# Performance work log

Hardware: AMD Instinct MI355X
Metric: run time of the kernel (lower is better)

## Reference

```python
import jax, jax.numpy as jnp
import numpy as np

B, S, T, DIN, DM, H = 4, 2048, 2048, 256, 512, 8
DH = DM // H
NEG = float(-2**32 + 1)
EPS = 1e-6


def layer_norm(x, g, b):
    mu = jnp.mean(x, axis=-1, keepdims=True)
    var = jnp.mean(jnp.square(x - mu), axis=-1, keepdims=True)
    return (x - mu) * jax.lax.rsqrt(var + EPS) * g + b


def mha(q_in, k_in, v_in, key_mask, wq, bq, wk, bk, wv, bv, w2, b2, g, beta, masked):
    b_, sq, _ = q_in.shape
    sk = k_in.shape[1]
    Q = (q_in @ wq + bq).reshape(b_, sq, H, DH)
    K = (k_in @ wk + bk).reshape(b_, sk, H, DH)
    V = (v_in @ wv + bv).reshape(b_, sk, H, DH)
    scores = jnp.einsum('bqhd,bkhd->bhqk', Q, K) / jnp.sqrt(jnp.float32(DH))
    if masked:
        m = key_mask.astype(jnp.float32).reshape(b_, 1, 1, sk)  # [B,1,1,Tk]
        scores = jnp.where(m == 0, jnp.float32(NEG), scores)
    attn = jax.nn.softmax(scores, axis=-1)  # dropout = identity at inference
    out = jnp.einsum('bhqk,bkhd->bqhd', attn, V).reshape(b_, sq, DM)
    out = out @ w2 + b2 + q_in
    return layer_norm(out, g, beta)


def setup_inputs() -> dict:
    key = jax.random.key(0)
    ks = jax.random.split(key, 16)
    w = lambda k, shp: (jax.random.normal(k, shp, jnp.float32) * 0.02)
    d = {
        'x': jax.random.normal(ks[0], (B, S, DIN), jnp.float32),
        'encoder_output': jax.random.normal(ks[1], (B, T, DIN), jnp.float32),
        'tgt_mask': jax.random.randint(ks[2], (B, S, 1), 0, 2, jnp.int32),
        'src_mask': jax.random.randint(ks[3], (B, T, 1), 0, 2, jnp.int32),
        'm1_wq': w(ks[4], (DIN, DM)), 'm1_bq': jnp.zeros((DM,), jnp.float32),
        'm1_wk': w(ks[5], (DIN, DM)), 'm1_bk': jnp.zeros((DM,), jnp.float32),
        'm1_wv': w(ks[6], (DIN, DM)), 'm1_bv': jnp.zeros((DM,), jnp.float32),
        'm1_w2': w(ks[7], (DM, DIN)), 'm1_b2': jnp.zeros((DIN,), jnp.float32),
        'm1_g': jnp.ones((DIN,), jnp.float32), 'm1_b': jnp.zeros((DIN,), jnp.float32),
        'm2_wq': w(ks[8], (DIN, DM)), 'm2_bq': jnp.zeros((DM,), jnp.float32),
        'm2_wk': w(ks[9], (DIN, DM)), 'm2_bk': jnp.zeros((DM,), jnp.float32),
        'm2_wv': w(ks[10], (DIN, DM)), 'm2_bv': jnp.zeros((DM,), jnp.float32),
        'm2_w2': w(ks[11], (DM, DIN)), 'm2_b2': jnp.zeros((DIN,), jnp.float32),
        'm2_g': jnp.ones((DIN,), jnp.float32), 'm2_b': jnp.zeros((DIN,), jnp.float32),
        'ln1_g': jnp.ones((DIN,), jnp.float32), 'ln1_b': jnp.zeros((DIN,), jnp.float32),
        'ln2_g': jnp.ones((DIN,), jnp.float32), 'ln2_b': jnp.zeros((DIN,), jnp.float32),
        'ln3_g': jnp.ones((DIN,), jnp.float32), 'ln3_b': jnp.zeros((DIN,), jnp.float32),
        'ffn_w1': w(ks[12], (DIN, DM)), 'ffn_b1': jnp.zeros((DM,), jnp.float32),
        'ffn_w2': w(ks[13], (DM, DIN)), 'ffn_b2': jnp.zeros((DIN,), jnp.float32),
    }
    return d


def reference(x, encoder_output, tgt_mask, src_mask,
              m1_wq, m1_bq, m1_wk, m1_bk, m1_wv, m1_bv, m1_w2, m1_b2, m1_g, m1_b,
              m2_wq, m2_bq, m2_wk, m2_bk, m2_wv, m2_bv, m2_w2, m2_b2, m2_g, m2_b,
              ln1_g, ln1_b, ln2_g, ln2_b, ln3_g, ln3_b,
              ffn_w1, ffn_b1, ffn_w2, ffn_b2):
    attn1 = mha(x, x, x, tgt_mask, m1_wq, m1_bq, m1_wk, m1_bk, m1_wv, m1_bv,
                m1_w2, m1_b2, m1_g, m1_b, masked=True)
    x = layer_norm(x + attn1, ln1_g, ln1_b)
    attn2 = mha(x, encoder_output, encoder_output, src_mask,
                m2_wq, m2_bq, m2_wk, m2_bk, m2_wv, m2_bv,
                m2_w2, m2_b2, m2_g, m2_b, masked=False)
    x = layer_norm(x + attn2, ln2_g, ln2_b)
    ffn_out = jax.nn.relu(x @ ffn_w1 + ffn_b1) @ ffn_w2 + ffn_b2
    return layer_norm(x + ffn_out, ln3_g, ln3_b)
```

## Files before the change

### kernel.cpp

```cpp
#include <hip/hip_runtime.h>
#include <hip/hip_bf16.h>

#define B_ 4
#define S_ 2048
#define DIN_ 256
#define DM_ 512
#define H_ 8
#define DH_ 64
#define M_ (B_*S_)

typedef short bf16x8 __attribute__((ext_vector_type(8)));
typedef float f32x4 __attribute__((ext_vector_type(4)));
typedef float f32x16 __attribute__((ext_vector_type(16)));
typedef int v2i __attribute__((ext_vector_type(2)));
typedef unsigned int u32;
typedef unsigned long long u64;

#define MFMA16(a,b,c) __builtin_amdgcn_mfma_f32_16x16x32_bf16((a),(b),(c),0,0,0)
#define MFMA32(a,b,c) __builtin_amdgcn_mfma_f32_32x32x16_bf16((a),(b),(c),0,0,0)

__device__ __forceinline__ unsigned short f2bf(float f) {
  union { float f; unsigned u; } v; v.f = f;
  unsigned r = v.u + 0x7fffu + ((v.u >> 16) & 1u);
  return (unsigned short)(r >> 16);
}
__device__ __forceinline__ f32x4 f32x4_zero() { f32x4 v = {0.f,0.f,0.f,0.f}; return v; }
__device__ __forceinline__ f32x16 f32x16_zero() {
  f32x16 v;
#pragma unroll
  for (int i = 0; i < 16; ++i) v[i] = 0.f;
  return v;
}
__device__ __forceinline__ u32 cvtpk_bf16(float lo, float hi) {
  u32 r; asm("v_cvt_pk_bf16_f32 %0, %1, %2" : "=v"(r) : "v"(lo), "v"(hi)); return r;
}
__device__ __forceinline__ float exp2_asm(float x) {
  float r; asm("v_exp_f32 %0, %1" : "=v"(r) : "v"(x)); return r;
}
__device__ __forceinline__ float max3f(float a, float b, float c) {
  return fmaxf(fmaxf(a, b), c);
}
__device__ __forceinline__ void gload_lds16(const void* g, void* l) {
  __builtin_amdgcn_global_load_lds((const __attribute__((address_space(1))) unsigned int*)g,
                                   (__attribute__((address_space(3))) unsigned int*)l,
                                   16, 0, 0);
}

__global__ void cast_bf16_kernel(const float* __restrict__ in,
                                 unsigned short* __restrict__ out, int n4) {
  int i = blockIdx.x * blockDim.x + threadIdx.x;
  if (i < n4) {
    float4 v = ((const float4*)in)[i];
    ushort4 o;
    o.x = f2bf(v.x); o.y = f2bf(v.y); o.z = f2bf(v.z); o.w = f2bf(v.w);
    ((ushort4*)out)[i] = o;
  }
}

struct WtDesc {
  const float* src[10];
  unsigned short* dst[10];
  int ks[10];
};
__global__ void prep_w_kernel(WtDesc d) {
  int m = blockIdx.y;
  int ks = d.ks[m];
  int K = 1 << ks;
  int N = 131072 >> ks;
  int i = blockIdx.x * 256 + threadIdx.x;
  int n = i >> ks, k = i & (K - 1);
  d.dst[m][i] = f2bf(d.src[m][(size_t)k * N + n]);
}

template<int K, bool RELU>
__global__ __launch_bounds__(256) void gemm_tiled_kernel(
    const unsigned short* __restrict__ A,
    const unsigned short* __restrict__ W0, const unsigned short* __restrict__ W1,
    const unsigned short* __restrict__ W2,
    const float* __restrict__ b0, const float* __restrict__ b1, const float* __restrict__ b2,
    unsigned short* __restrict__ o0, unsigned short* __restrict__ o1,
    unsigned short* __restrict__ o2, float scale0) {
  const int sel = blockIdx.y >> 2;
  const unsigned short* Wt = sel == 0 ? W0 : (sel == 1 ? W1 : W2);
  const float* bias = sel == 0 ? b0 : (sel == 1 ? b1 : b2);
  unsigned short* out = sel == 0 ? o0 : (sel == 1 ? o1 : o2);
  const float scale = sel == 0 ? scale0 : 1.f;

  const int tid = threadIdx.x;
  const int w = tid >> 6, l = tid & 63;
  const int lr = l & 15, lg = l >> 4;
  const int wr = w >> 1, wc = w & 1;
  const int r0 = blockIdx.x * 128;
  const int c0 = (blockIdx.y & 3) * 128;

  __shared__ __align__(16) unsigned short As[2][128 * 32];
  __shared__ __align__(16) unsigned short Bs[2][128 * 32];

  f32x4 acc[4][4];
#pragma unroll
  for (int m = 0; m < 4; ++m)
#pragma unroll
    for (int n = 0; n < 4; ++n) acc[m][n] = f32x4_zero();

  auto stage = [&](int buf, int k0) {
#pragma unroll
    for (int i = 0; i < 2; ++i) {
      int c = w * 128 + i * 64 + l;
      int row = c >> 2, sl = c & 3;
      gload_lds16(A + (size_t)(r0 + row) * K + k0 + sl * 8,
                  &As[buf][(w * 128 + i * 64) * 8]);
      gload_lds16(Wt + (size_t)(c0 + row) * K + k0 + sl * 8,
                  &Bs[buf][(w * 128 + i * 64) * 8]);
    }
  };

  stage(0, 0);
  __syncthreads();

  const int NT = K / 32;
  for (int t = 0; t < NT; ++t) {
    if (t + 1 < NT) stage((t + 1) & 1, (t + 1) * 32);
    const unsigned short* AB = &As[t & 1][0];
    const unsigned short* BB = &Bs[t & 1][0];
    bf16x8 af[4], bf[4];
#pragma unroll
    for (int m = 0; m < 4; ++m)
      af[m] = *(const bf16x8*)&AB[(wr * 64 + m * 16 + lr) * 32 + lg * 8];
#pragma unroll
    for (int n = 0; n < 4; ++n)
      bf[n] = *(const bf16x8*)&BB[(wc * 64 + n * 16 + lr) * 32 + lg * 8];
#pragma unroll
    for (int m = 0; m < 4; ++m)
#pragma unroll
      for (int n = 0; n < 4; ++n)
        acc[m][n] = MFMA16(af[m], bf[n], acc[m][n]);
    __syncthreads();
  }

#pragma unroll
  for (int n = 0; n < 4; ++n) {
    int col = c0 + wc * 64 + n * 16 + lr;
    float bv = bias[col];
#pragma unroll
    for (int m = 0; m < 4; ++m) {
#pragma unroll
      for (int r = 0; r < 4; ++r) {
        int row = r0 + wr * 64 + m * 16 + lg * 4 + r;
        float v = (acc[m][n][r] + bv) * scale;
        if (RELU) v = fmaxf(v, 0.f);
        out[(size_t)row * DM_ + col] = f2bf(v);
      }
    }
  }
}

template<int NLN>
__global__ __launch_bounds__(256) void gemm_ln_kernel(
    const unsigned short* __restrict__ A,
    const unsigned short* __restrict__ Wt,
    const float* __restrict__ bias,
    const float* __restrict__ res,
    const float* __restrict__ gA, const float* __restrict__ bA,
    const float* __restrict__ gB, const float* __restrict__ bB,
    float* __restrict__ outF,
    unsigned short* __restrict__ outB) {
  const int tid = threadIdx.x;
  const int w = tid >> 6, l = tid & 63;
  const int lr = l & 15, lg = l >> 4;
  const int wh = w & 1, wv = w >> 1;
  const int r0 = blockIdx.x * 32;

  __shared__ __align__(16) unsigned short Bs[2][256 * 32];
  __shared__ __align__(16) unsigned short As[2][32 * 32];
  __shared__ float ex[32][2][2];

  f32x4 acc[8];
#pragma unroll
  for (int n = 0; n < 8; ++n) acc[n] = f32x4_zero();

  auto stage = [&](int buf, int k0) {
#pragma unroll
    for (int i = 0; i < 4; ++i) {
      int c = w * 256 + i * 64 + l;
      int row = c >> 2, sl = c & 3;
      gload_lds16(Wt + (size_t)row * 512 + k0 + sl * 8,
                  &Bs[buf][(w * 256 + i * 64) * 8]);
    }
    if (w < 2) {
      int c = w * 64 + l;
      int row = c >> 2, sl = c & 3;
      gload_lds16(A + (size_t)(r0 + row) * 512 + k0 + sl * 8,
                  &As[buf][w * 64 * 8]);
    }
  };

  stage(0, 0);
  __syncthreads();

  for (int t = 0; t < 16; ++t) {
    if (t + 1 < 16) stage((t + 1) & 1, (t + 1) * 32);
    const unsigned short* BB = &Bs[t & 1][0];
    const unsigned short* AB = &As[t & 1][0];
    bf16x8 a = *(const bf16x8*)&AB[(wv * 16 + lr) * 32 + lg * 8];
#pragma unroll
    for (int n = 0; n < 8; ++n) {
      bf16x8 b = *(const bf16x8*)&BB[(wh * 128 + n * 16 + lr) * 32 + lg * 8];
      acc[n] = MFMA16(a, b, acc[n]);
    }
    __syncthreads();
  }

  f32x4 rv[8];
#pragma unroll
  for (int n = 0; n < 8; ++n) {
    int col = wh * 128 + n * 16 + lr;
    float bv = bias[col];
#pragma unroll
    for (int r = 0; r < 4; ++r) {
      int row = r0 + wv * 16 + lg * 4 + r;
      float rr = res[(size_t)row * 256 + col];
      rv[n][r] = rr;
      acc[n][r] += bv + rr;
    }
  }

  float mu[4], rs[4];
  {
    float s1[4], s2[4];
#pragma unroll
    for (int r = 0; r < 4; ++r) {
      float a1 = 0.f, a2 = 0.f;
#pragma unroll
      for (int n = 0; n < 8; ++n) { float v = acc[n][r]; a1 += v; a2 += v * v; }
#pragma unroll
      for (int off = 1; off < 16; off <<= 1) {
        a1 += __shfl_xor(a1, off);
        a2 += __shfl_xor(a2, off);
      }
      s1[r] = a1; s2[r] = a2;
    }
    if (lr == 0) {
#pragma unroll
      for (int r = 0; r < 4; ++r) {
        ex[wv * 16 + lg * 4 + r][wh][0] = s1[r];
        ex[wv * 16 + lg * 4 + r][wh][1] = s2[r];
      }
    }
    __syncthreads();
#pragma unroll
    for (int r = 0; r < 4; ++r) {
      int row = wv * 16 + lg * 4 + r;
      float t1 = ex[row][0][0] + ex[row][1][0];
      float t2 = ex[row][0][1] + ex[row][1][1];
      float m = t1 * (1.f / 256.f);
      float var = t2 * (1.f / 256.f) - m * m;
      mu[r] = m;
      rs[r] = rsqrtf(var + 1e-6f);
    }
  }

  if constexpr (NLN == 2) {
#pragma unroll
    for (int n = 0; n < 8; ++n) {
      int col = wh * 128 + n * 16 + lr;
      float g = gA[col], bb = bA[col];
#pragma unroll
      for (int r = 0; r < 4; ++r) {
        float t1 = (acc[n][r] - mu[r]) * rs[r] * g + bb;
        acc[n][r] = rv[n][r] + t1;
      }
    }
    float mu2[4], rs2[4];
    {
      float s1[4], s2[4];
#pragma unroll
      for (int r = 0; r < 4; ++r) {
        float a1 = 0.f, a2 = 0.f;
#pragma unroll
        for (int n = 0; n < 8; ++n) { float v = acc[n][r]; a1 += v; a2 += v * v; }
#pragma unroll
        for (int off = 1; off < 16; off <<= 1) {
          a1 += __shfl_xor(a1, off);
          a2 += __shfl_xor(a2, off);
        }
        s1[r] = a1; s2[r] = a2;
      }
      __syncthreads();
      if (lr == 0) {
#pragma unroll
        for (int r = 0; r < 4; ++r) {
          ex[wv * 16 + lg * 4 + r][wh][0] = s1[r];
          ex[wv * 16 + lg * 4 + r][wh][1] = s2[r];
        }
      }
      __syncthreads();
#pragma unroll
      for (int r = 0; r < 4; ++r) {
        int row = wv * 16 + lg * 4 + r;
        float t1 = ex[row][0][0] + ex[row][1][0];
        float t2 = ex[row][0][1] + ex[row][1][1];
        float m = t1 * (1.f / 256.f);
        float var = t2 * (1.f / 256.f) - m * m;
        mu2[r] = m;
        rs2[r] = rsqrtf(var + 1e-6f);
      }
    }
#pragma unroll
    for (int n = 0; n < 8; ++n) {
      int col = wh * 128 + n * 16 + lr;
      float g = gB[col], bb = bB[col];
#pragma unroll
      for (int r = 0; r < 4; ++r) {
        int row = r0 + wv * 16 + lg * 4 + r;
        float o = (acc[n][r] - mu2[r]) * rs2[r] * g + bb;
        outF[(size_t)row * 256 + col] = o;
        outB[(size_t)row * 256 + col] = f2bf(o);
      }
    }
  } else {
#pragma unroll
    for (int n = 0; n < 8; ++n) {
      int col = wh * 128 + n * 16 + lr;
      float g = gA[col], bb = bA[col];
#pragma unroll
      for (int r = 0; r < 4; ++r) {
        int row = r0 + wv * 16 + lg * 4 + r;
        float o = (acc[n][r] - mu[r]) * rs[r] * g + bb;
        outF[(size_t)row * 256 + col] = o;
      }
    }
  }
}

__global__ __launch_bounds__(256) void trans_kernel(const unsigned short* __restrict__ V,
                                                    unsigned short* __restrict__ Vt) {
  __shared__ __align__(16) unsigned short T[64][72];
  int v = threadIdx.x;
  int b = blockIdx.z;
  int s0 = blockIdx.x * 64, c0 = blockIdx.y * 64;
#pragma unroll
  for (int it = 0; it < 2; ++it) {
    int r = (v >> 3) + it * 32, c8 = (v & 7) * 8;
    *(bf16x8*)&T[r][c8] = *(const bf16x8*)&V[((size_t)b * S_ + s0 + r) * DM_ + c0 + c8];
  }
  __syncthreads();
#pragma unroll
  for (int it = 0; it < 2; ++it) {
    int cr = (v >> 3) + it * 32, s8 = (v & 7) * 8;
    bf16x8 o;
#pragma unroll
    for (int j = 0; j < 8; ++j) o[j] = (short)T[s8 + j][cr];
    *(bf16x8*)&Vt[((size_t)b * DM_ + c0 + cr) * S_ + s0 + s8] = o;
  }
}

template<bool MASKED>
__global__ __launch_bounds__(256) void flash_kernel(
    const unsigned short* __restrict__ Q,
    const unsigned short* __restrict__ Kg,
    const unsigned short* __restrict__ Vt,
    const int* __restrict__ mask,
    unsigned short* __restrict__ O) {
  __shared__ __align__(16) unsigned short lds[2][2][64 * 64];
  const int tid = threadIdx.x;
  const int w = tid >> 6, l = tid & 63;
  const int q32 = l & 31, hi = l >> 5;
  const int id = blockIdx.x;
  const int g = (id & 7) * 64 + (id >> 3);
  const int bh = g >> 4, xblk = g & 15;
  const int b = bh >> 3, h = bh & 7;
  const size_t bS = (size_t)b * S_;
  const int q0 = xblk * 128 + w * 32;

  bf16x8 qf[4];
  {
    const unsigned short* qp = Q + (bS + q0 + q32) * DM_ + h * DH_;
#pragma unroll
    for (int c = 0; c < 4; ++c) qf[c] = *(const bf16x8*)(qp + c * 16 + hi * 8);
  }
  bf16x8 ones;
#pragma unroll
  for (int j = 0; j < 8; ++j) ones[j] = (short)0x3F80;

  f32x16 o0 = f32x16_zero(), o1 = f32x16_zero();
  float m = -1e30f, lsum = 0.f;

  auto stage = [&](int buf, int kv0) {
#pragma unroll
    for (int p = 0; p < 2; ++p) {
      int i = w * 2 + p;
      int row = i * 8 + (l >> 3);
      int slot = l & 7;
      gload_lds16(Kg + (bS + kv0 + row) * DM_ + h * DH_ + ((slot ^ (row & 7)) * 8),
                  &lds[buf][0][i * 8 * 64]);
      gload_lds16(Vt + ((size_t)b * DM_ + h * DH_ + row) * S_ + kv0 + ((slot ^ (row & 7)) * 8),
                  &lds[buf][1][i * 8 * 64]);
    }
  };

  stage(0, 0);
  int mvCur = 1;
  if (MASKED) mvCur = mask[bS + l];
  __syncthreads();

  const int NT = S_ / 64;
  for (int tt = 0; tt < NT; tt += 2) {
#pragma unroll
    for (int u = 0; u < 2; ++u) {
      const int t = tt + u;
      int mvNext = 1;
      if (t + 1 < NT) {
        stage(u ^ 1, (t + 1) * 64);
        if (MASKED) mvNext = mask[bS + (t + 1) * 64 + l];
      }
      u64 bits = 0;
      if (MASKED) bits = __ballot(mvCur != 0);

      const unsigned short* KB = &lds[u][0][0];
      const unsigned short* VB = &lds[u][1][0];

      f32x16 sc[2];
      __builtin_amdgcn_s_setprio(1);
#pragma unroll
      for (int kt = 0; kt < 2; ++kt) {
        f32x16 s = f32x16_zero();
#pragma unroll
        for (int c = 0; c < 4; ++c) {
          int row = kt * 32 + q32;
          int slot = (c * 2 + hi) ^ (row & 7);
          bf16x8 kf = *(const bf16x8*)&KB[row * 64 + slot * 8];
          s = MFMA32(kf, qf[c], s);
        }
        if (MASKED) {
          u32 valid = (u32)(bits >> (kt * 32 + q32)) & 1u;
          u32 mfw = valid ? 0u : 0xC080C080u;
          union { u32 u[4]; bf16x8 v; } mf;
          mf.u[0] = mfw; mf.u[1] = mfw; mf.u[2] = mfw; mf.u[3] = mfw;
          s = MFMA32(mf.v, ones, s);
        }
        sc[kt] = s;
      }
      __builtin_amdgcn_s_setprio(0);

      float tm;
      {
        float r01;
#pragma unroll
        for (int kt = 0; kt < 2; ++kt) {
          float m0 = max3f(sc[kt][0], sc[kt][1], sc[kt][2]);
          float m1 = max3f(sc[kt][3], sc[kt][4], sc[kt][5]);
          float m2 = max3f(sc[kt][6], sc[kt][7], sc[kt][8]);
          float m3 = max3f(sc[kt][9], sc[kt][10], sc[kt][11]);
          float m4 = max3f(sc[kt][12], sc[kt][13], sc[kt][14]);
          float r = fmaxf(max3f(max3f(m0, m1, m2), m3, m4), sc[kt][15]);
          if (kt == 0) r01 = r; else r01 = fmaxf(r01, r);
        }
        tm = fmaxf(r01, __shfl_xor(r01, 32));
      }

      if (__any(tm > m + 11.5f)) {
        float mn = fmaxf(m, tm);
        float fac = exp2_asm(m - mn);
        m = mn;
        lsum *= fac;
#pragma unroll
        for (int i = 0; i < 16; ++i) {
          int rq = (i & 3) + 8 * (i >> 2) + 4 * hi;
          float fr = __shfl(fac, rq);
          o0[i] *= fr;
          o1[i] *= fr;
        }
      }

      float pv[2][16];
#pragma unroll
      for (int kt = 0; kt < 2; ++kt)
#pragma unroll
        for (int i = 0; i < 16; ++i) pv[kt][i] = exp2_asm(sc[kt][i] - m);

      {
        float s0 = 0.f, s1 = 0.f, s2 = 0.f, s3 = 0.f;
#pragma unroll
        for (int kt = 0; kt < 2; ++kt)
#pragma unroll
          for (int i = 0; i < 16; i += 4) {
            s0 += pv[kt][i]; s1 += pv[kt][i + 1];
            s2 += pv[kt][i + 2]; s3 += pv[kt][i + 3];
          }
        float rsum = (s0 + s1) + (s2 + s3);
        rsum += __shfl_xor(rsum, 32);
        lsum += rsum;
      }

      u32 w8[2][8];
#pragma unroll
      for (int kt = 0; kt < 2; ++kt)
#pragma unroll
        for (int j = 0; j < 8; ++j)
          w8[kt][j] = cvtpk_bf16(pv[kt][2 * j], pv[kt][2 * j + 1]);

      __builtin_amdgcn_s_setprio(1);
#pragma unroll
      for (int kt = 0; kt < 2; ++kt) {
#pragma unroll
        for (int kc = 0; kc < 2; ++kc) {
          v2i r0 = __builtin_amdgcn_permlane32_swap((int)w8[kt][4 * kc + 0],
                                                    (int)w8[kt][4 * kc + 2], false, false);
          v2i r1 = __builtin_amdgcn_permlane32_swap((int)w8[kt][4 * kc + 1],
                                                    (int)w8[kt][4 * kc + 3], false, false);
          union { u32 u[4]; bf16x8 v; } af;
          af.u[0] = (u32)r0.x; af.u[1] = (u32)r1.x; af.u[2] = (u32)r0.y; af.u[3] = (u32)r1.y;
          {
            int row = q32;
            int slot = (kt * 4 + kc * 2 + hi) ^ (row & 7);
            bf16x8 vf = *(const bf16x8*)&VB[row * 64 + slot * 8];
            o0 = MFMA32(af.v, vf, o0);
          }
          {
            int row = 32 + q32;
            int slot = (kt * 4 + kc * 2 + hi) ^ (row & 7);
            bf16x8 vf = *(const bf16x8*)&VB[row * 64 + slot * 8];
            o1 = MFMA32(af.v, vf, o1);
          }
        }
      }
      __builtin_amdgcn_s_setprio(0);
      __syncthreads();
      mvCur = mvNext;
    }
  }

#pragma unroll
  for (int i = 0; i < 16; ++i) {
    int rq = (i & 3) + 8 * (i >> 2) + 4 * hi;
    float ls = __shfl(lsum, rq);
    float inv = __builtin_amdgcn_rcpf(ls);
    int row = q0 + rq;
    O[(bS + row) * DM_ + h * DH_ + q32] = f2bf(o0[i] * inv);
    O[(bS + row) * DM_ + h * DH_ + 32 + q32] = f2bf(o1[i] * inv);
  }
}

extern "C" void kernel_launch(void* const* d_in, const int* in_sizes, int n_in,
                              void* d_out, int out_size, void* d_ws, size_t ws_size,
                              hipStream_t stream) {
  const float* x     = (const float*)d_in[0];
  const float* eo    = (const float*)d_in[1];
  const int*   tmask = (const int*)d_in[2];
  const float* m1_wq = (const float*)d_in[4];  const float* m1_bq = (const float*)d_in[5];
  const float* m1_wk = (const float*)d_in[6];  const float* m1_bk = (const float*)d_in[7];
  const float* m1_wv = (const float*)d_in[8];  const float* m1_bv = (const float*)d_in[9];
  const float* m1_w2 = (const float*)d_in[10]; const float* m1_b2 = (const float*)d_in[11];
  const float* m1_g  = (const float*)d_in[12]; const float* m1_b  = (const float*)d_in[13];
  const float* m2_wq = (const float*)d_in[14]; const float* m2_bq = (const float*)d_in[15];
  const float* m2_wk = (const float*)d_in[16]; const float* m2_bk = (const float*)d_in[17];
  const float* m2_wv = (const float*)d_in[18]; const float* m2_bv = (const float*)d_in[19];
  const float* m2_w2 = (const float*)d_in[20]; const float* m2_b2 = (const float*)d_in[21];
  const float* m2_g  = (const float*)d_in[22]; const float* m2_b  = (const float*)d_in[23];
  const float* ln1_g = (const float*)d_in[24]; const float* ln1_b = (const float*)d_in[25];
  const float* ln2_g = (const float*)d_in[26]; const float* ln2_b = (const float*)d_in[27];
  const float* ln3_g = (const float*)d_in[28]; const float* ln3_b = (const float*)d_in[29];
  const float* f_w1  = (const float*)d_in[30]; const float* f_b1  = (const float*)d_in[31];
  const float* f_w2  = (const float*)d_in[32]; const float* f_b2  = (const float*)d_in[33];

  char* ws = (char*)d_ws;
  size_t off = 0;
  auto alloc = [&](size_t bytes) -> void* {
    void* p = ws + off;
    off += (bytes + 255) & ~(size_t)255;
    return p;
  };
  unsigned short* wt[10];
  for (int i = 0; i < 10; ++i) wt[i] = (unsigned short*)alloc(131072 * 2);
  unsigned short* xb  = (unsigned short*)alloc((size_t)M_ * DIN_ * 2);
  unsigned short* eb  = (unsigned short*)alloc((size_t)M_ * DIN_ * 2);
  unsigned short* Qb  = (unsigned short*)alloc((size_t)M_ * DM_ * 2);
  unsigned short* Kb  = (unsigned short*)alloc((size_t)M_ * DM_ * 2);
  unsigned short* Vb  = (unsigned short*)alloc((size_t)M_ * DM_ * 2);
  unsigned short* AOb = (unsigned short*)alloc((size_t)M_ * DM_ * 2);
  float*          X1  = (float*)alloc((size_t)M_ * DIN_ * 4);
  unsigned short* X1b = (unsigned short*)alloc((size_t)M_ * DIN_ * 2);
  float*          X2  = (float*)alloc((size_t)M_ * DIN_ * 4);
  unsigned short* X2b = (unsigned short*)alloc((size_t)M_ * DIN_ * 2);
  unsigned short* Hb  = Qb;
  unsigned short* VtA = (unsigned short*)X2;
  unsigned short* VtB = xb;

  int n4 = M_ * DIN_ / 4;
  cast_bf16_kernel<<<n4 / 256, 256, 0, stream>>>(x, xb, n4);
  cast_bf16_kernel<<<n4 / 256, 256, 0, stream>>>(eo, eb, n4);

  WtDesc wd;
  const float* srcs[10] = {m1_wq, m1_wk, m1_wv, m1_w2, m2_wq, m2_wk, m2_wv, m2_w2, f_w1, f_w2};
  int kss[10]           = {8,     8,     8,     9,     8,     8,     8,     9,     8,    9};
  for (int i = 0; i < 10; ++i) { wd.src[i] = srcs[i]; wd.dst[i] = wt[i]; wd.ks[i] = kss[i]; }
  prep_w_kernel<<<dim3(512, 10), 256, 0, stream>>>(wd);

  dim3 tg(S_ / 64, DM_ / 64, B_);
  const int FG = (S_ / 128) * H_ * B_;
  const float QSCALE = 0.125f * 1.44269504088896f;

  gemm_tiled_kernel<256, false><<<dim3(M_ / 128, 12), 256, 0, stream>>>(
      xb, wt[0], wt[1], wt[2], m1_bq, m1_bk, m1_bv, Qb, Kb, Vb, QSCALE);
  trans_kernel<<<tg, 256, 0, stream>>>(Vb, VtA);
  flash_kernel<true><<<FG, 256, 0, stream>>>(Qb, Kb, VtA, tmask, AOb);
  gemm_ln_kernel<2><<<M_ / 32, 256, 0, stream>>>(AOb, wt[3], m1_b2, x,
                                                 m1_g, m1_b, ln1_g, ln1_b, X1, X1b);
  gemm_tiled_kernel<256, false><<<dim3(M_ / 128, 4), 256, 0, stream>>>(
      X1b, wt[4], wt[4], wt[4], m2_bq, m2_bq, m2_bq, Qb, Qb, Qb, QSCALE);
  gemm_tiled_kernel<256, false><<<dim3(M_ / 128, 8), 256, 0, stream>>>(
      eb, wt[5], wt[6], wt[6], m2_bk, m2_bv, m2_bv, Kb, Vb, Vb, 1.f);
  trans_kernel<<<tg, 256, 0, stream>>>(Vb, VtB);
  flash_kernel<false><<<FG, 256, 0, stream>>>(Qb, Kb, VtB, nullptr, AOb);
  gemm_ln_kernel<2><<<M_ / 32, 256, 0, stream>>>(AOb, wt[7], m2_b2, X1,
                                                 m2_g, m2_b, ln2_g, ln2_b, X2, X2b);
  gemm_tiled_kernel<256, true><<<dim3(M_ / 128, 4), 256, 0, stream>>>(
      X2b, wt[8], wt[8], wt[8], f_b1, f_b1, f_b1, Hb, Hb, Hb, 1.f);
  gemm_ln_kernel<1><<<M_ / 32, 256, 0, stream>>>(Hb, wt[9], f_b2, X2,
                                                 ln3_g, ln3_b, nullptr, nullptr,
                                                 (float*)d_out, nullptr);
}
```

Measured before the change: 223.3 us.

## Software-pipeline QK^T one tile ahead with four-deep LDS ring buffer

Restructures the flash attention loop so the QK^T MFMAs for tile t+1 are issued before the softmax and PV work of tile t. K/V staging now runs two tiles ahead using a 4-slot LDS ring instead of double buffering. The aim is to overlap matrix-core work with the exp/max/sum VALU work and to hide global load latency better. The cost is doubled LDS use (64KB per block) and an extra live score accumulator set, which may reduce occupancy or add register pressure.

After: 247.8 us. 1.11x slower.

```diff
diff --git a/kernel.cpp b/kernel.cpp
--- a/kernel.cpp
+++ b/kernel.cpp
@@ -361,7 +361,7 @@
     const unsigned short* __restrict__ Vt,
     const int* __restrict__ mask,
     unsigned short* __restrict__ O) {
-  __shared__ __align__(16) unsigned short lds[2][2][64 * 64];
+  __shared__ __align__(16) unsigned short lds[4][2][64 * 64];
   const int tid = threadIdx.x;
   const int w = tid >> 6, l = tid & 63;
   const int q32 = l & 31, hi = l >> 5;
@@ -384,6 +384,9 @@
 
   f32x16 o0 = f32x16_zero(), o1 = f32x16_zero();
   float m = -1e30f, lsum = 0.f;
+  int mvQ = 1;
+
+  const int NT = S_ / 64;
 
   auto stage = [&](int buf, int kv0) {
 #pragma unroll
@@ -398,136 +401,135 @@
     }
   };
 
+  auto qkt = [&](const unsigned short* KB, u64 bits, f32x16* dst) {
+    __builtin_amdgcn_s_setprio(1);
+#pragma unroll
+    for (int kt = 0; kt < 2; ++kt) {
+      f32x16 s = f32x16_zero();
+#pragma unroll
+      for (int c = 0; c < 4; ++c) {
+        int row = kt * 32 + q32;
+        int slot = (c * 2 + hi) ^ (row & 7);
+        bf16x8 kf = *(const bf16x8*)&KB[row * 64 + slot * 8];
+        s = MFMA32(kf, qf[c], s);
+      }
+      if (MASKED) {
+        u32 valid = (u32)(bits >> (kt * 32 + q32)) & 1u;
+        u32 mfw = valid ? 0u : 0xC080C080u;
+        union { u32 u[4]; bf16x8 v; } mf;
+        mf.u[0] = mfw; mf.u[1] = mfw; mf.u[2] = mfw; mf.u[3] = mfw;
+        s = MFMA32(mf.v, ones, s);
+      }
+      dst[kt] = s;
+    }
+    __builtin_amdgcn_s_setprio(0);
+  };
+
+  auto body = [&](int t, f32x16* cur, f32x16* nxt) {
+    if (t + 2 < NT) stage((t + 2) & 3, (t + 2) * 64);
+    if (t + 1 < NT) {
+      u64 bitsQ = 0;
+      if (MASKED) bitsQ = __ballot(mvQ != 0);
+      qkt(&lds[(t + 1) & 3][0][0], bitsQ, nxt);
+      if (MASKED && t + 2 < NT) mvQ = mask[bS + (t + 2) * 64 + l];
+    }
+    float tm;
+    {
+      float r01;
+#pragma unroll
+      for (int kt = 0; kt < 2; ++kt) {
+        float m0 = max3f(cur[kt][0], cur[kt][1], cur[kt][2]);
+        float m1 = max3f(cur[kt][3], cur[kt][4], cur[kt][5]);
+        float m2 = max3f(cur[kt][6], cur[kt][7], cur[kt][8]);
+        float m3 = max3f(cur[kt][9], cur[kt][10], cur[kt][11]);
+        float m4 = max3f(cur[kt][12], cur[kt][13], cur[kt][14]);
+        float r = fmaxf(max3f(max3f(m0, m1, m2), m3, m4), cur[kt][15]);
+        if (kt == 0) r01 = r; else r01 = fmaxf(r01, r);
+      }
+      tm = fmaxf(r01, __shfl_xor(r01, 32));
+    }
+    if (__any(tm > m + 11.5f)) {
+      float mn = fmaxf(m, tm);
+      float fac = exp2_asm(m - mn);
+      m = mn;
+      lsum *= fac;
+#pragma unroll
+      for (int i = 0; i < 16; ++i) {
+        int rq = (i & 3) + 8 * (i >> 2) + 4 * hi;
+        float fr = __shfl(fac, rq);
+        o0[i] *= fr;
+        o1[i] *= fr;
+      }
+    }
+#pragma unroll
+    for (int kt = 0; kt < 2; ++kt)
+#pragma unroll
+      for (int i = 0; i < 16; ++i) cur[kt][i] = exp2_asm(cur[kt][i] - m);
+    {
+      float s0 = 0.f, s1 = 0.f, s2 = 0.f, s3 = 0.f;
+#pragma unroll
+      for (int kt = 0; kt < 2; ++kt)
+#pragma unroll
+        for (int i = 0; i < 16; i += 4) {
+          s0 += cur[kt][i]; s1 += cur[kt][i + 1];
+          s2 += cur[kt][i + 2]; s3 += cur[kt][i + 3];
+        }
+      float rsum = (s0 + s1) + (s2 + s3);
+      rsum += __shfl_xor(rsum, 32);
+      lsum += rsum;
+    }
+    u32 w8[2][8];
+#pragma unroll
+    for (int kt = 0; kt < 2; ++kt)
+#pragma unroll
+      for (int j = 0; j < 8; ++j)
+        w8[kt][j] = cvtpk_bf16(cur[kt][2 * j], cur[kt][2 * j + 1]);
+
+    const unsigned short* VB = &lds[t & 3][1][0];
+    __builtin_amdgcn_s_setprio(1);
+#pragma unroll
+    for (int kt = 0; kt < 2; ++kt) {
+#pragma unroll
+      for (int kc = 0; kc < 2; ++kc) {
+        v2i r0 = __builtin_amdgcn_permlane32_swap((int)w8[kt][4 * kc + 0],
+                                                  (int)w8[kt][4 * kc + 2], false, false);
+        v2i r1 = __builtin_amdgcn_permlane32_swap((int)w8[kt][4 * kc + 1],
+                                                  (int)w8[kt][4 * kc + 3], false, false);
+        union { u32 u[4]; bf16x8 v; } af;
+        af.u[0] = (u32)r0.x; af.u[1] = (u32)r1.x; af.u[2] = (u32)r0.y; af.u[3] = (u32)r1.y;
+        {
+          int row = q32;
+          int slot = (kt * 4 + kc * 2 + hi) ^ (row & 7);
+          bf16x8 vf = *(const bf16x8*)&VB[row * 64 + slot * 8];
+          o0 = MFMA32(af.v, vf, o0);
+        }
+        {
+          int row = 32 + q32;
+          int slot = (kt * 4 + kc * 2 + hi) ^ (row & 7);
+          bf16x8 vf = *(const bf16x8*)&VB[row * 64 + slot * 8];
+          o1 = MFMA32(af.v, vf, o1);
+        }
+      }
+    }
+    __builtin_amdgcn_s_setprio(0);
+    __syncthreads();
+  };
+
   stage(0, 0);
-  int mvCur = 1;
-  if (MASKED) mvCur = mask[bS + l];
+  stage(1, 64);
+  int mv0 = 1;
+  if (MASKED) { mv0 = mask[bS + l]; mvQ = mask[bS + 64 + l]; }
   __syncthreads();
-
-  const int NT = S_ / 64;
+  f32x16 scA[2], scB[2];
+  {
+    u64 bits0 = 0;
+    if (MASKED) bits0 = __ballot(mv0 != 0);
+    qkt(&lds[0][0][0], bits0, scA);
+  }
+
   for (int tt = 0; tt < NT; tt += 2) {
-#pragma unroll
-    for (int u = 0; u < 2; ++u) {
-      const int t = tt + u;
-      int mvNext = 1;
-      if (t + 1 < NT) {
-        stage(u ^ 1, (t + 1) * 64);
-        if (MASKED) mvNext = mask[bS + (t + 1) * 64 + l];
-      }
-      u64 bits = 0;
-      if (MASKED) bits = __ballot(mvCur != 0);
-
-      const unsigned short* KB = &lds[u][0][0];
-      const unsigned short* VB = &lds[u][1][0];
-
-      f32x16 sc[2];
-      __builtin_amdgcn_s_setprio(1);
-#pragma unroll
-      for (int kt = 0; kt < 2; ++kt) {
-        f32x16 s = f32x16_zero();
-#pragma unroll
-        for (int c = 0; c < 4; ++c) {
-          int row = kt * 32 + q32;
-          int slot = (c * 2 + hi) ^ (row & 7);
-          bf16x8 kf = *(const bf16x8*)&KB[row * 64 + slot * 8];
-          s = MFMA32(kf, qf[c], s);
-        }
-        if (MASKED) {
-          u32 valid = (u32)(bits >> (kt * 32 + q32)) & 1u;
-          u32 mfw = valid ? 0u : 0xC080C080u;
-          union { u32 u[4]; bf16x8 v; } mf;
-          mf.u[0] = mfw; mf.u[1] = mfw; mf.u[2] = mfw; mf.u[3] = mfw;
-          s = MFMA32(mf.v, ones, s);
-        }
-        sc[kt] = s;
-      }
-      __builtin_amdgcn_s_setprio(0);
-
-      float tm;
-      {
-        float r01;
-#pragma unroll
-        for (int kt = 0; kt < 2; ++kt) {
-          float m0 = max3f(sc[kt][0], sc[kt][1], sc[kt][2]);
-          float m1 = max3f(sc[kt][3], sc[kt][4], sc[kt][5]);
-          float m2 = max3f(sc[kt][6], sc[kt][7], sc[kt][8]);
-          float m3 = max3f(sc[kt][9], sc[kt][10], sc[kt][11]);
-          float m4 = max3f(sc[kt][12], sc[kt][13], sc[kt][14]);
-          float r = fmaxf(max3f(max3f(m0, m1, m2), m3, m4), sc[kt][15]);
-          if (kt == 0) r01 = r; else r01 = fmaxf(r01, r);
-        }
-        tm = fmaxf(r01, __shfl_xor(r01, 32));
-      }
-
-      if (__any(tm > m + 11.5f)) {
-        float mn = fmaxf(m, tm);
-        float fac = exp2_asm(m - mn);
-        m = mn;
-        lsum *= fac;
-#pragma unroll
-        for (int i = 0; i < 16; ++i) {
-          int rq = (i & 3) + 8 * (i >> 2) + 4 * hi;
-          float fr = __shfl(fac, rq);
-          o0[i] *= fr;
-          o1[i] *= fr;
-        }
-      }
-
-      float pv[2][16];
-#pragma unroll
-      for (int kt = 0; kt < 2; ++kt)
-#pragma unroll
-        for (int i = 0; i < 16; ++i) pv[kt][i] = exp2_asm(sc[kt][i] - m);
-
-      {
-        float s0 = 0.f, s1 = 0.f, s2 = 0.f, s3 = 0.f;
-#pragma unroll
-        for (int kt = 0; kt < 2; ++kt)
-#pragma unroll
-          for (int i = 0; i < 16; i += 4) {
-            s0 += pv[kt][i]; s1 += pv[kt][i + 1];
-            s2 += pv[kt][i + 2]; s3 += pv[kt][i + 3];
-          }
-        float rsum = (s0 + s1) + (s2 + s3);
-        rsum += __shfl_xor(rsum, 32);
-        lsum += rsum;
-      }
-
-      u32 w8[2][8];
-#pragma unroll
-      for (int kt = 0; kt < 2; ++kt)
-#pragma unroll
-        for (int j = 0; j < 8; ++j)
-          w8[kt][j] = cvtpk_bf16(pv[kt][2 * j], pv[kt][2 * j + 1]);
-
-      __builtin_amdgcn_s_setprio(1);
-#pragma unroll
-      for (int kt = 0; kt < 2; ++kt) {
-#pragma unroll
-        for (int kc = 0; kc < 2; ++kc) {
-          v2i r0 = __builtin_amdgcn_permlane32_swap((int)w8[kt][4 * kc + 0],
-                                                    (int)w8[kt][4 * kc + 2], false, false);
-          v2i r1 = __builtin_amdgcn_permlane32_swap((int)w8[kt][4 * kc + 1],
-                                                    (int)w8[kt][4 * kc + 3], false, false);
-          union { u32 u[4]; bf16x8 v; } af;
-          af.u[0] = (u32)r0.x; af.u[1] = (u32)r1.x; af.u[2] = (u32)r0.y; af.u[3] = (u32)r1.y;
-          {
-            int row = q32;
-            int slot = (kt * 4 + kc * 2 + hi) ^ (row & 7);
-            bf16x8 vf = *(const bf16x8*)&VB[row * 64 + slot * 8];
-            o0 = MFMA32(af.v, vf, o0);
-          }
-          {
-            int row = 32 + q32;
-            int slot = (kt * 4 + kc * 2 + hi) ^ (row & 7);
-            bf16x8 vf = *(const bf16x8*)&VB[row * 64 + slot * 8];
-            o1 = MFMA32(af.v, vf, o1);
-          }
-        }
-      }
-      __builtin_amdgcn_s_setprio(0);
-      __syncthreads();
-      mvCur = mvNext;
-    }
+    body(tt,     scA, scB);
+    body(tt + 1, scB, scA);
   }
 
 #pragma unroll
```
